# Kernel tuning notes

Measured on AMD Instinct MI355X. Metric: run time of the kernel, lower is better.

## Reference

```python
import jax, jax.numpy as jnp
import numpy as np

# ---- instant-ngp style multi-resolution hash-grid config (matches torch-ngp HashEncoder) ----
NUM_LEVELS = 16
LEVEL_DIM = 2
BASE_RES = 16
DESIRED_RES = 2048
LOG2_T = 19
T_MAX = 2 ** LOG2_T
_pls = np.exp2(np.log2(DESIRED_RES / BASE_RES) / (NUM_LEVELS - 1))  # per-level scale ~1.3819
RESOLUTIONS = [int(np.ceil(BASE_RES * _pls ** l)) for l in range(NUM_LEVELS)]
LEVEL_SIZES = [min(T_MAX, int(np.ceil((r + 1) ** 3 / 8) * 8)) for r in RESOLUTIONS]
OFFSETS = np.concatenate([[0], np.cumsum(LEVEL_SIZES)]).astype(np.int64)
TOTAL_PARAMS = int(OFFSETS[-1])
HASHED = [(r + 1) ** 3 > T_MAX for r in RESOLUTIONS]
CORNERS = np.array([[i, j, k] for i in (0, 1) for j in (0, 1) for k in (0, 1)], dtype=np.float32)  # [8,3]

N_POINTS = 524288
MULTIRES = 6  # positional embedding freqs -> input_ch = 3 + 3*2*6 = 39
D_IN0 = 3 + MULTIRES * 6 + NUM_LEVELS * LEVEL_DIM  # 71


def hash_encode(x, table):
    """x: [N,3] in [0,1]; table: [TOTAL_PARAMS, LEVEL_DIM] -> [N, NUM_LEVELS*LEVEL_DIM]."""
    cn = jnp.asarray(CORNERS)              # [8,3]
    cn_u = cn.astype(jnp.uint32)
    p1, p2, p3 = jnp.uint32(1), jnp.uint32(2654435761), jnp.uint32(805459861)
    outs = []
    for l in range(NUM_LEVELS):
        res = RESOLUTIONS[l]
        pos = x * jnp.float32(res - 1)     # [N,3]
        p0 = jnp.floor(pos)
        w = pos - p0                        # [N,3] trilinear fractions
        cpos = p0.astype(jnp.uint32)[:, None, :] + cn_u[None]  # [N,8,3] corner coords
        if HASHED[l]:
            idx = (cpos[..., 0] * p1) ^ (cpos[..., 1] * p2) ^ (cpos[..., 2] * p3)
            idx = (idx % jnp.uint32(LEVEL_SIZES[l])).astype(jnp.int32)
        else:
            stride = jnp.uint32(res + 1)
            idx = (cpos[..., 0] + cpos[..., 1] * stride + cpos[..., 2] * stride * stride).astype(jnp.int32)
        feats = table[int(OFFSETS[l]) + idx]  # [N,8,LEVEL_DIM] irregular gather
        cw = jnp.where(cn[None] == 1.0, w[:, None, :], 1.0 - w[:, None, :])  # [N,8,3]
        wgt = cw[..., 0] * cw[..., 1] * cw[..., 2]  # [N,8]
        outs.append(jnp.einsum('nc,ncd->nd', wgt, feats))  # [N,LEVEL_DIM]
    return jnp.concatenate(outs, axis=-1)


def pos_embed(x):
    # NeRF embedder, include_input=True, log-sampled freqs 2^0..2^(MULTIRES-1), sin/cos
    freqs = jnp.asarray(2.0 ** np.arange(MULTIRES), dtype=x.dtype)   # [6]
    ang = x[:, None, :] * freqs[None, :, None]                        # [N,6,3]
    sc = jnp.stack([jnp.sin(ang), jnp.cos(ang)], axis=2)              # [N,6,2,3]
    return jnp.concatenate([x, sc.reshape(x.shape[0], -1)], axis=-1)  # [N,39]


def linear_wn(x, v, g, b):
    # nn.utils.weight_norm: W = g * v / ||v||_row
    Wn = v * (g / jnp.linalg.norm(v, axis=1))[:, None]
    return x @ Wn.T + b


def softplus100(x):
    # nn.Softplus(beta=100)
    return jax.nn.softplus(100.0 * x) * 0.01


def setup_inputs() -> dict:
    key = jax.random.key(0)
    ks = jax.random.split(key, 8)
    x = jax.random.uniform(ks[0], (N_POINTS, 3), dtype=jnp.float32)
    hash_table = jax.random.uniform(ks[1], (TOTAL_PARAMS, LEVEL_DIM), jnp.float32, -1e-4, 1e-4)

    def lin(k, dout, din):
        v = jax.random.normal(k, (dout, din), jnp.float32) * jnp.float32(np.sqrt(2.0 / dout))
        g = jnp.linalg.norm(v, axis=1)  # weight_norm init: g = ||v||
        b = jnp.zeros((dout,), jnp.float32)
        return v, g, b

    v0, g0, b0 = lin(ks[2], 256, D_IN0)   # 71 -> 256
    v1, g1, b1 = lin(ks[3], 256, 256)     # 256 -> 256
    v2, g2, b2 = lin(ks[4], 257, 256)     # 256 -> 1 + feature_vector_size
    return {"x": x, "hash_table": hash_table,
            "v0": v0, "g0": g0, "b0": b0,
            "v1": v1, "g1": g1, "b1": b1,
            "v2": v2, "g2": g2, "b2": b2}


def reference(x, hash_table, v0, g0, b0, v1, g1, b1, v2, g2, b2):
    # ImplicitNetworkGrid.forward (divide_factor = 1.0, use_grid_feature = True)
    feat = hash_encode(x, hash_table)                    # [N,32]
    h = jnp.concatenate([pos_embed(x), feat], axis=-1)   # [N,71] = cat(embed, feature)
    h = softplus100(linear_wn(h, v0, g0, b0))
    h = softplus100(linear_wn(h, v1, g1, b1))
    return linear_wn(h, v2, g2, b2)                      # [N,257]: sdf + feature vector
```

## Files before the change

### kernel.cpp

```cpp
#include <hip/hip_runtime.h>
#include <cmath>

typedef float f32x4 __attribute__((ext_vector_type(4)));
typedef short short8 __attribute__((ext_vector_type(8)));

#define N_POINTS 524288
#define TMASK 0x7FFFFu
#define NCELLS 32768

struct HashCfg { int res[16]; int off[16]; unsigned hashed_mask; int total; };

#define S0_OFF   0
#define S1_OFF   1024
#define S2_OFF   2048
#define W2L_OFF  3328
#define B0_OFF   4608
#define B1_OFF   (B0_OFF + 49152)
#define B2_OFF   (B1_OFF + 131072)
#define TBF_OFF  (B2_OFF + 131072)

__device__ inline unsigned short f2bf(float f){
  unsigned u = __float_as_uint(f);
  u = (u + 0x7FFFu + ((u >> 16) & 1u)) >> 16;
  return (unsigned short)u;
}
__device__ inline float bf2f(unsigned short h){
  return __uint_as_float(((unsigned)h) << 16);
}
__device__ inline float softplus100_fast(float x){
  float y = 100.f * x;
  return 0.01f * (fmaxf(y, 0.f) + __logf(1.f + __expf(-fabsf(y))));
}
__device__ inline unsigned morton5(unsigned cx, unsigned cy, unsigned cz){
  unsigned k = 0;
  #pragma unroll
  for (int b = 0; b < 5; b++){
    k |= ((cx >> b) & 1u) << (3*b)
       | ((cy >> b) & 1u) << (3*b + 1)
       | ((cz >> b) & 1u) << (3*b + 2);
  }
  return k;
}

__global__ void scale_kernel(const float* __restrict__ v0, const float* __restrict__ g0,
                             const float* __restrict__ v1, const float* __restrict__ g1,
                             const float* __restrict__ v2, const float* __restrict__ g2,
                             char* __restrict__ ws){
  int r = blockIdx.x * 256 + threadIdx.x;
  if (r < 256){
    float s = 0.f;
    for (int k = 0; k < 71; k++){ float t = v0[r*71+k]; s += t*t; }
    ((float*)(ws + S0_OFF))[r] = g0[r] / sqrtf(s);
  } else if (r < 512){
    int o = r - 256; float s = 0.f;
    for (int k = 0; k < 256; k++){ float t = v1[o*256+k]; s += t*t; }
    ((float*)(ws + S1_OFF))[o] = g1[o] / sqrtf(s);
  } else if (r < 769){
    int o = r - 512; float s = 0.f;
    for (int k = 0; k < 256; k++){ float t = v2[o*256+k]; s += t*t; }
    ((float*)(ws + S2_OFF))[o] = g2[o] / sqrtf(s);
  }
}

__global__ void pack_kernel(const float* __restrict__ v0, const float* __restrict__ v1,
                            const float* __restrict__ v2, char* __restrict__ ws){
  int i = blockIdx.x * 256 + threadIdx.x;
  const float* s0 = (const float*)(ws + S0_OFF);
  const float* s1 = (const float*)(ws + S1_OFF);
  const float* s2 = (const float*)(ws + S2_OFF);
  if (i < 24576){
    int j = i & 7, l = (i >> 3) & 63, q = i >> 9;
    int kt = q % 3, nt = q / 3;
    int k = kt*32 + (l >> 4)*8 + j, col = nt*16 + (l & 15);
    float v = (k < 71) ? v0[col*71 + k] * s0[col] : 0.f;
    ((unsigned short*)(ws + B0_OFF))[i] = f2bf(v);
  } else if (i < 90112){
    int e = i - 24576;
    int j = e & 7, l = (e >> 3) & 63, q = e >> 9;
    int kt = q & 7, nt = q >> 3;
    int k = kt*32 + (l >> 4)*8 + j, col = nt*16 + (l & 15);
    ((unsigned short*)(ws + B1_OFF))[e] = f2bf(v1[col*256 + k] * s1[col]);
  } else if (i < 155648){
    int e = i - 90112;
    int j = e & 7, l = (e >> 3) & 63, q = e >> 9;
    int kt = q & 7, nt = q >> 3;
    int k = kt*32 + (l >> 4)*8 + j, col = nt*16 + (l & 15);
    ((unsigned short*)(ws + B2_OFF))[e] = f2bf(v2[col*256 + k] * s2[col]);
  } else if (i < 155904){
    int k = i - 155648;
    ((float*)(ws + W2L_OFF))[k] = v2[256*256 + k] * s2[256];
  }
}

__global__ void tconv_kernel(const float* __restrict__ table, char* __restrict__ ws, int total){
  int i = blockIdx.x * 256 + threadIdx.x;
  if (i < total){
    float2 v = ((const float2*)table)[i];
    unsigned lo = ((unsigned)f2bf(v.x));
    unsigned hi = ((unsigned)f2bf(v.y)) << 16;
    ((unsigned*)(ws + TBF_OFF))[i] = lo | hi;
  }
}

__global__ void hist_kernel(const float* __restrict__ xin,
                            unsigned* __restrict__ hist, unsigned* __restrict__ keys){
  int i = blockIdx.x * 256 + threadIdx.x;
  float x0 = xin[i*3], x1 = xin[i*3+1], x2 = xin[i*3+2];
  unsigned cx = min(31u, (unsigned)(x0 * 32.f));
  unsigned cy = min(31u, (unsigned)(x1 * 32.f));
  unsigned cz = min(31u, (unsigned)(x2 * 32.f));
  unsigned k = morton5(cx, cy, cz);
  keys[i] = k;
  atomicAdd(&hist[k], 1u);
}

__global__ __launch_bounds__(1024) void scan_kernel(unsigned* __restrict__ hist){
  __shared__ unsigned sdata[1024];
  int t = threadIdx.x;
  unsigned loc[32];
  unsigned s = 0;
  #pragma unroll
  for (int k = 0; k < 32; k++){ loc[k] = hist[t*32 + k]; s += loc[k]; }
  sdata[t] = s;
  __syncthreads();
  for (int d = 1; d < 1024; d <<= 1){
    unsigned v = (t >= d) ? sdata[t - d] : 0u;
    __syncthreads();
    sdata[t] += v;
    __syncthreads();
  }
  unsigned run = (t == 0) ? 0u : sdata[t - 1];
  #pragma unroll
  for (int k = 0; k < 32; k++){ unsigned c = loc[k]; hist[t*32 + k] = run; run += c; }
}

__global__ void scatter_kernel(const unsigned* __restrict__ keys,
                               unsigned* __restrict__ hist, int* __restrict__ perm){
  int i = blockIdx.x * 256 + threadIdx.x;
  unsigned k = keys[i];
  unsigned r = atomicAdd(&hist[k], 1u);
  perm[r] = i;
}

template<int USEBF>
__global__ __launch_bounds__(256, 4) void fused3(
    const float* __restrict__ xin, const float* __restrict__ table,
    char* __restrict__ ws, const int* __restrict__ perm,
    const float* __restrict__ b0, const float* __restrict__ b1, const float* __restrict__ b2,
    float* __restrict__ out, HashCfg cfg)
{
  __shared__ unsigned short buf[64 * 256];
  __shared__ float colsc[4][64];
  __shared__ int pids[64];

  const int tid = threadIdx.x;
  const int p   = tid & 63;
  const int grp = tid >> 6;
  const int lb  = (blockIdx.x & 7) * 1024 + (blockIdx.x >> 3);
  const int idx = lb * 64 + p;
  const int pid = perm ? perm[idx] : idx;
  if (grp == 0) pids[p] = pid;

  const float x0 = xin[pid*3], x1 = xin[pid*3+1], x2 = xin[pid*3+2];
  const unsigned* __restrict__ tbf = (const unsigned*)(ws + TBF_OFF);

  auto stB = [&](int row, int col, float v){
    buf[row*256 + (col ^ ((row & 7) << 3))] = f2bf(v);
  };
  auto ldB = [&](int row, int kb) -> short8 {
    return *(const short8*)&buf[row*256 + (kb ^ ((row & 7) << 3))];
  };

  {
    float wxa[4], wya[4], wza[4];
    unsigned vb[4][8];
    float2   vf2[4][8];

    #pragma unroll
    for (int ii = 0; ii < 4; ii++){
      int lev = grp*4 + ii;
      int res = cfg.res[lev];
      float scl = (float)(res - 1);
      float px = x0*scl, py = x1*scl, pz = x2*scl;
      float fx = floorf(px), fy = floorf(py), fz = floorf(pz);
      wxa[ii] = px - fx; wya[ii] = py - fy; wza[ii] = pz - fz;
      unsigned cx0 = (unsigned)fx, cy0 = (unsigned)fy, cz0 = (unsigned)fz;
      unsigned r1 = (unsigned)(res + 1);
      bool hl = (cfg.hashed_mask >> lev) & 1;
      unsigned base = (unsigned)cfg.off[lev];
      #pragma unroll
      for (int c = 0; c < 8; c++){
        unsigned bx = (c >> 2) & 1, by = (c >> 1) & 1, bz = c & 1;
        unsigned cx = cx0 + bx, cy = cy0 + by, cz = cz0 + bz;
        unsigned hidx = hl ? ((cx ^ (cy * 2654435761u) ^ (cz * 805459861u)) & TMASK)
                           : (cx + cy * r1 + cz * r1 * r1);
        if (USEBF) vb[ii][c]  = tbf[base + hidx];
        else       vf2[ii][c] = *(const float2*)(table + (size_t)(base + hidx) * 2u);
      }
    }

    if (grp < 3){
      float xv[3] = {x0, x1, x2};
      #pragma unroll
      for (int fi = 0; fi < 2; fi++){
        int f = grp*2 + fi;
        float fr = (float)(1 << f);
        #pragma unroll
        for (int d = 0; d < 3; d++){
          float a = xv[d] * fr;
          stB(p, 3 + f*6 + d,     __sinf(a));
          stB(p, 3 + f*6 + 3 + d, __cosf(a));
        }
      }
    } else {
      stB(p, 0, x0); stB(p, 1, x1); stB(p, 2, x2);
      #pragma unroll
      for (int c = 71; c < 96; c++)
        buf[p*256 + (c ^ ((p & 7) << 3))] = 0;
    }

    #pragma unroll
    for (int ii = 0; ii < 4; ii++){
      int lev = grp*4 + ii;
      float wx = wxa[ii], wy = wya[ii], wz = wza[ii];
      float f0 = 0.f, f1 = 0.f;
      #pragma unroll
      for (int c = 0; c < 8; c++){
        unsigned bx = (c >> 2) & 1, by = (c >> 1) & 1, bz = c & 1;
        float w = (bx ? wx : 1.f - wx) * (by ? wy : 1.f - wy) * (bz ? wz : 1.f - wz);
        if (USEBF){
          unsigned u = vb[ii][c];
          f0 += w * __uint_as_float(u << 16);
          f1 += w * __uint_as_float(u & 0xffff0000u);
        } else {
          f0 += w * vf2[ii][c].x;
          f1 += w * vf2[ii][c].y;
        }
      }
      stB(p, 39 + 2*lev, f0);
      stB(p, 40 + 2*lev, f1);
    }
  }
  __syncthreads();

  const int l  = tid & 63;
  const int lr = l & 15;
  const int lh = l >> 4;
  const int wv = grp;
  const short8* B0p = (const short8*)(ws + B0_OFF);
  const short8* B1p = (const short8*)(ws + B1_OFF);
  const short8* B2p = (const short8*)(ws + B2_OFF);

  {
    f32x4 acc[4][4];
    #pragma unroll
    for (int a = 0; a < 4; a++)
      #pragma unroll
      for (int b = 0; b < 4; b++) acc[a][b] = (f32x4){0.f,0.f,0.f,0.f};
    #pragma unroll
    for (int kt = 0; kt < 3; kt++){
      short8 af[4];
      #pragma unroll
      for (int mt = 0; mt < 4; mt++) af[mt] = ldB(mt*16 + lr, kt*32 + lh*8);
      #pragma unroll
      for (int nt = 0; nt < 4; nt++){
        short8 bf = B0p[((wv*4 + nt)*3 + kt)*64 + l];
        #pragma unroll
        for (int mt = 0; mt < 4; mt++)
          acc[mt][nt] = __builtin_amdgcn_mfma_f32_16x16x32_bf16(af[mt], bf, acc[mt][nt], 0, 0, 0);
      }
    }
    __syncthreads();
    float bb[4];
    #pragma unroll
    for (int nt = 0; nt < 4; nt++) bb[nt] = b0[wv*64 + nt*16 + lr];
    #pragma unroll
    for (int mt = 0; mt < 4; mt++)
      #pragma unroll
      for (int nt = 0; nt < 4; nt++){
        int c = wv*64 + nt*16 + lr;
        #pragma unroll
        for (int j = 0; j < 4; j++)
          stB(mt*16 + lh*4 + j, c, softplus100_fast(acc[mt][nt][j] + bb[nt]));
      }
  }
  __syncthreads();

  {
    f32x4 acc[4][4];
    #pragma unroll
    for (int a = 0; a < 4; a++)
      #pragma unroll
      for (int b = 0; b < 4; b++) acc[a][b] = (f32x4){0.f,0.f,0.f,0.f};
    #pragma unroll
    for (int kt = 0; kt < 8; kt++){
      short8 af[4];
      #pragma unroll
      for (int mt = 0; mt < 4; mt++) af[mt] = ldB(mt*16 + lr, kt*32 + lh*8);
      #pragma unroll
      for (int nt = 0; nt < 4; nt++){
        short8 bf = B1p[((wv*4 + nt)*8 + kt)*64 + l];
        #pragma unroll
        for (int mt = 0; mt < 4; mt++)
          acc[mt][nt] = __builtin_amdgcn_mfma_f32_16x16x32_bf16(af[mt], bf, acc[mt][nt], 0, 0, 0);
      }
    }
    __syncthreads();
    float bb[4];
    #pragma unroll
    for (int nt = 0; nt < 4; nt++) bb[nt] = b1[wv*64 + nt*16 + lr];
    #pragma unroll
    for (int mt = 0; mt < 4; mt++)
      #pragma unroll
      for (int nt = 0; nt < 4; nt++){
        int c = wv*64 + nt*16 + lr;
        #pragma unroll
        for (int j = 0; j < 4; j++)
          stB(mt*16 + lh*4 + j, c, softplus100_fast(acc[mt][nt][j] + bb[nt]));
      }
  }
  __syncthreads();

  {
    const float* w2l = (const float*)(ws + W2L_OFF);
    float s = 0.f;
    #pragma unroll
    for (int q = 0; q < 8; q++){
      short8 h = ldB(l, wv*64 + q*8);
      #pragma unroll
      for (int j = 0; j < 8; j++)
        s += bf2f((unsigned short)h[j]) * w2l[wv*64 + q*8 + j];
    }
    colsc[wv][l] = s;
  }

  {
    f32x4 acc[4][4];
    #pragma unroll
    for (int a = 0; a < 4; a++)
      #pragma unroll
      for (int b = 0; b < 4; b++) acc[a][b] = (f32x4){0.f,0.f,0.f,0.f};
    #pragma unroll
    for (int kt = 0; kt < 8; kt++){
      short8 af[4];
      #pragma unroll
      for (int mt = 0; mt < 4; mt++) af[mt] = ldB(mt*16 + lr, kt*32 + lh*8);
      #pragma unroll
      for (int nt = 0; nt < 4; nt++){
        short8 bf = B2p[((wv*4 + nt)*8 + kt)*64 + l];
        #pragma unroll
        for (int mt = 0; mt < 4; mt++)
          acc[mt][nt] = __builtin_amdgcn_mfma_f32_16x16x32_bf16(af[mt], bf, acc[mt][nt], 0, 0, 0);
      }
    }
    __syncthreads();
    float bb[4];
    #pragma unroll
    for (int nt = 0; nt < 4; nt++) bb[nt] = b2[wv*64 + nt*16 + lr];
    int rowid[4][4];
    #pragma unroll
    for (int mt = 0; mt < 4; mt++)
      #pragma unroll
      for (int j = 0; j < 4; j++) rowid[mt][j] = pids[mt*16 + lh*4 + j];
    #pragma unroll
    for (int mt = 0; mt < 4; mt++)
      #pragma unroll
      for (int nt = 0; nt < 4; nt++){
        int c = wv*64 + nt*16 + lr;
        #pragma unroll
        for (int j = 0; j < 4; j++)
          out[(size_t)rowid[mt][j]*257 + c] = acc[mt][nt][j] + bb[nt];
      }
    if (tid < 64)
      out[(size_t)pids[tid]*257 + 256] =
        colsc[0][tid] + colsc[1][tid] + colsc[2][tid] + colsc[3][tid] + b2[256];
  }
}

static HashCfg make_cfg(){
  HashCfg c;
  double pls = exp2(log2(2048.0 / 16.0) / 15.0);
  long long off = 0;
  unsigned mask = 0;
  for (int l = 0; l < 16; l++){
    int r = (int)ceil(16.0 * pow(pls, (double)l));
    c.res[l] = r;
    c.off[l] = (int)off;
    double n3 = (double)(r + 1) * (double)(r + 1) * (double)(r + 1);
    long long size;
    if (n3 > 524288.0){ mask |= (1u << l); }
    size = (long long)(ceil(n3 / 8.0) * 8.0);
    if (size > 524288) size = 524288;
    off += size;
  }
  c.hashed_mask = mask;
  c.total = (int)off;
  return c;
}

extern "C" void kernel_launch(void* const* d_in, const int* in_sizes, int n_in,
                              void* d_out, int out_size, void* d_ws, size_t ws_size,
                              hipStream_t stream) {
  const float* x     = (const float*)d_in[0];
  const float* table = (const float*)d_in[1];
  const float* v0 = (const float*)d_in[2];
  const float* g0 = (const float*)d_in[3];
  const float* b0 = (const float*)d_in[4];
  const float* v1 = (const float*)d_in[5];
  const float* g1 = (const float*)d_in[6];
  const float* b1 = (const float*)d_in[7];
  const float* v2 = (const float*)d_in[8];
  const float* g2 = (const float*)d_in[9];
  const float* b2 = (const float*)d_in[10];
  float* out = (float*)d_out;
  char* ws = (char*)d_ws;

  HashCfg cfg = make_cfg();
  size_t tbf_bytes = (size_t)cfg.total * 4u;
  size_t hist_off  = (TBF_OFF + tbf_bytes + 255) & ~(size_t)255;
  size_t keys_off  = hist_off + (size_t)NCELLS * 4;
  size_t perm_off  = keys_off + (size_t)N_POINTS * 4;
  size_t need_sort = perm_off + (size_t)N_POINTS * 4;
  size_t need_bf   = TBF_OFF + tbf_bytes;

  hipLaunchKernelGGL(scale_kernel, dim3(4), dim3(256), 0, stream, v0, g0, v1, g1, v2, g2, ws);
  hipLaunchKernelGGL(pack_kernel, dim3(609), dim3(256), 0, stream, v0, v1, v2, ws);

  if (ws_size >= need_sort){
    unsigned* hist = (unsigned*)(ws + hist_off);
    unsigned* keys = (unsigned*)(ws + keys_off);
    int*      perm = (int*)(ws + perm_off);
    hipMemsetAsync(hist, 0, (size_t)NCELLS * 4, stream);
    hipLaunchKernelGGL(tconv_kernel, dim3((cfg.total + 255) / 256), dim3(256), 0, stream,
                       table, ws, cfg.total);
    hipLaunchKernelGGL(hist_kernel, dim3(N_POINTS / 256), dim3(256), 0, stream, x, hist, keys);
    hipLaunchKernelGGL(scan_kernel, dim3(1), dim3(1024), 0, stream, hist);
    hipLaunchKernelGGL(scatter_kernel, dim3(N_POINTS / 256), dim3(256), 0, stream, keys, hist, perm);
    hipLaunchKernelGGL((fused3<1>), dim3(N_POINTS / 64), dim3(256), 0, stream,
                       x, table, ws, perm, b0, b1, b2, out, cfg);
  } else if (ws_size >= need_bf){
    hipLaunchKernelGGL(tconv_kernel, dim3((cfg.total + 255) / 256), dim3(256), 0, stream,
                       table, ws, cfg.total);
    hipLaunchKernelGGL((fused3<1>), dim3(N_POINTS / 64), dim3(256), 0, stream,
                       x, table, ws, (const int*)nullptr, b0, b1, b2, out, cfg);
  } else {
    hipLaunchKernelGGL((fused3<0>), dim3(N_POINTS / 64), dim3(256), 0, stream,
                       x, table, ws, (const int*)nullptr, b0, b1, b2, out, cfg);
  }
}
```

Baseline: 789.1 us.

## Process four 64-point tiles per block with prefetched hash gathers

```diff
diff --git a/kernel.cpp b/kernel.cpp
--- a/kernel.cpp
+++ b/kernel.cpp
@@ -7,6 +7,7 @@
 #define N_POINTS 524288
 #define TMASK 0x7FFFFu
 #define NCELLS 32768
+#define TILES  4
 
 struct HashCfg { int res[16]; int off[16]; unsigned hashed_mask; int total; };
 
@@ -96,9 +97,7 @@
   int i = blockIdx.x * 256 + threadIdx.x;
   if (i < total){
     float2 v = ((const float2*)table)[i];
-    unsigned lo = ((unsigned)f2bf(v.x));
-    unsigned hi = ((unsigned)f2bf(v.y)) << 16;
-    ((unsigned*)(ws + TBF_OFF))[i] = lo | hi;
+    ((unsigned*)(ws + TBF_OFF))[i] = ((unsigned)f2bf(v.x)) | (((unsigned)f2bf(v.y)) << 16);
   }
 }
 
@@ -143,7 +142,7 @@
 }
 
 template<int USEBF>
-__global__ __launch_bounds__(256, 4) void fused3(
+__global__ __launch_bounds__(256, 3) void fused4(
     const float* __restrict__ xin, const float* __restrict__ table,
     char* __restrict__ ws, const int* __restrict__ perm,
     const float* __restrict__ b0, const float* __restrict__ b1, const float* __restrict__ b2,
@@ -151,18 +150,23 @@
 {
   __shared__ unsigned short buf[64 * 256];
   __shared__ float colsc[4][64];
-  __shared__ int pids[64];
+  __shared__ int pids_sh[TILES][64];
 
   const int tid = threadIdx.x;
   const int p   = tid & 63;
   const int grp = tid >> 6;
-  const int lb  = (blockIdx.x & 7) * 1024 + (blockIdx.x >> 3);
-  const int idx = lb * 64 + p;
-  const int pid = perm ? perm[idx] : idx;
-  if (grp == 0) pids[p] = pid;
-
-  const float x0 = xin[pid*3], x1 = xin[pid*3+1], x2 = xin[pid*3+2];
+  const int l   = tid & 63;
+  const int lr  = l & 15;
+  const int lh  = l >> 4;
+  const int wv  = grp;
+  const int lb  = (blockIdx.x & 7) * 256 + (blockIdx.x >> 3);
+  const int base_idx = lb * (TILES * 64);
+
   const unsigned* __restrict__ tbf = (const unsigned*)(ws + TBF_OFF);
+  const short8* B0p = (const short8*)(ws + B0_OFF);
+  const short8* B1p = (const short8*)(ws + B1_OFF);
+  const short8* B2p = (const short8*)(ws + B2_OFF);
+  const float* w2l = (const float*)(ws + W2L_OFF);
 
   auto stB = [&](int row, int col, float v){
     buf[row*256 + (col ^ ((row & 7) << 3))] = f2bf(v);
@@ -171,17 +175,29 @@
     return *(const short8*)&buf[row*256 + (kb ^ ((row & 7) << 3))];
   };
 
-  {
-    float wxa[4], wya[4], wza[4];
-    unsigned vb[4][8];
-    float2   vf2[4][8];
-
+  if (grp == 0){
+    #pragma unroll
+    for (int t = 0; t < TILES; t++){
+      int gi = base_idx + t*64 + p;
+      pids_sh[t][p] = perm ? perm[gi] : gi;
+    }
+  }
+  __syncthreads();
+
+  float xc0, xc1, xc2;
+  float wxa[4], wya[4], wza[4];
+  unsigned vb[4][8];
+  float2   vf2[4][8];
+
+  auto issue_tile = [&](int t){
+    int pid = pids_sh[t][p];
+    xc0 = xin[pid*3]; xc1 = xin[pid*3+1]; xc2 = xin[pid*3+2];
     #pragma unroll
     for (int ii = 0; ii < 4; ii++){
       int lev = grp*4 + ii;
       int res = cfg.res[lev];
       float scl = (float)(res - 1);
-      float px = x0*scl, py = x1*scl, pz = x2*scl;
+      float px = xc0*scl, py = xc1*scl, pz = xc2*scl;
       float fx = floorf(px), fy = floorf(py), fz = floorf(pz);
       wxa[ii] = px - fx; wya[ii] = py - fy; wza[ii] = pz - fz;
       unsigned cx0 = (unsigned)fx, cy0 = (unsigned)fy, cz0 = (unsigned)fz;
@@ -198,27 +214,11 @@
         else       vf2[ii][c] = *(const float2*)(table + (size_t)(base + hidx) * 2u);
       }
     }
-
-    if (grp < 3){
-      float xv[3] = {x0, x1, x2};
-      #pragma unroll
-      for (int fi = 0; fi < 2; fi++){
-        int f = grp*2 + fi;
-        float fr = (float)(1 << f);
-        #pragma unroll
-        for (int d = 0; d < 3; d++){
-          float a = xv[d] * fr;
-          stB(p, 3 + f*6 + d,     __sinf(a));
-          stB(p, 3 + f*6 + 3 + d, __cosf(a));
-        }
-      }
-    } else {
-      stB(p, 0, x0); stB(p, 1, x1); stB(p, 2, x2);
-      #pragma unroll
-      for (int c = 71; c < 96; c++)
-        buf[p*256 + (c ^ ((p & 7) << 3))] = 0;
-    }
-
+  };
+
+  issue_tile(0);
+
+  for (int t = 0; t < TILES; t++){
     #pragma unroll
     for (int ii = 0; ii < 4; ii++){
       int lev = grp*4 + ii;
@@ -240,140 +240,152 @@
       stB(p, 39 + 2*lev, f0);
       stB(p, 40 + 2*lev, f1);
     }
-  }
-  __syncthreads();
-
-  const int l  = tid & 63;
-  const int lr = l & 15;
-  const int lh = l >> 4;
-  const int wv = grp;
-  const short8* B0p = (const short8*)(ws + B0_OFF);
-  const short8* B1p = (const short8*)(ws + B1_OFF);
-  const short8* B2p = (const short8*)(ws + B2_OFF);
-
-  {
-    f32x4 acc[4][4];
-    #pragma unroll
-    for (int a = 0; a < 4; a++)
-      #pragma unroll
-      for (int b = 0; b < 4; b++) acc[a][b] = (f32x4){0.f,0.f,0.f,0.f};
-    #pragma unroll
-    for (int kt = 0; kt < 3; kt++){
-      short8 af[4];
-      #pragma unroll
-      for (int mt = 0; mt < 4; mt++) af[mt] = ldB(mt*16 + lr, kt*32 + lh*8);
-      #pragma unroll
-      for (int nt = 0; nt < 4; nt++){
-        short8 bf = B0p[((wv*4 + nt)*3 + kt)*64 + l];
-        #pragma unroll
-        for (int mt = 0; mt < 4; mt++)
-          acc[mt][nt] = __builtin_amdgcn_mfma_f32_16x16x32_bf16(af[mt], bf, acc[mt][nt], 0, 0, 0);
-      }
-    }
+    if (grp < 3){
+      float xv[3] = {xc0, xc1, xc2};
+      #pragma unroll
+      for (int fi = 0; fi < 2; fi++){
+        int f = grp*2 + fi;
+        float fr = (float)(1 << f);
+        #pragma unroll
+        for (int d = 0; d < 3; d++){
+          float a = xv[d] * fr;
+          stB(p, 3 + f*6 + d,     __sinf(a));
+          stB(p, 3 + f*6 + 3 + d, __cosf(a));
+        }
+      }
+    } else {
+      stB(p, 0, xc0); stB(p, 1, xc1); stB(p, 2, xc2);
+      #pragma unroll
+      for (int c = 71; c < 96; c++)
+        buf[p*256 + (c ^ ((p & 7) << 3))] = 0;
+    }
+
+    if (t + 1 < TILES) issue_tile(t + 1);
     __syncthreads();
-    float bb[4];
-    #pragma unroll
-    for (int nt = 0; nt < 4; nt++) bb[nt] = b0[wv*64 + nt*16 + lr];
-    #pragma unroll
-    for (int mt = 0; mt < 4; mt++)
-      #pragma unroll
-      for (int nt = 0; nt < 4; nt++){
-        int c = wv*64 + nt*16 + lr;
-        #pragma unroll
-        for (int j = 0; j < 4; j++)
-          stB(mt*16 + lh*4 + j, c, softplus100_fast(acc[mt][nt][j] + bb[nt]));
-      }
-  }
-  __syncthreads();
-
-  {
-    f32x4 acc[4][4];
-    #pragma unroll
-    for (int a = 0; a < 4; a++)
-      #pragma unroll
-      for (int b = 0; b < 4; b++) acc[a][b] = (f32x4){0.f,0.f,0.f,0.f};
-    #pragma unroll
-    for (int kt = 0; kt < 8; kt++){
-      short8 af[4];
-      #pragma unroll
-      for (int mt = 0; mt < 4; mt++) af[mt] = ldB(mt*16 + lr, kt*32 + lh*8);
-      #pragma unroll
-      for (int nt = 0; nt < 4; nt++){
-        short8 bf = B1p[((wv*4 + nt)*8 + kt)*64 + l];
-        #pragma unroll
-        for (int mt = 0; mt < 4; mt++)
-          acc[mt][nt] = __builtin_amdgcn_mfma_f32_16x16x32_bf16(af[mt], bf, acc[mt][nt], 0, 0, 0);
-      }
+
+    {
+      f32x4 acc[4][4];
+      #pragma unroll
+      for (int a = 0; a < 4; a++)
+        #pragma unroll
+        for (int b = 0; b < 4; b++) acc[a][b] = (f32x4){0.f,0.f,0.f,0.f};
+      #pragma unroll
+      for (int kt = 0; kt < 3; kt++){
+        short8 af[4];
+        #pragma unroll
+        for (int mt = 0; mt < 4; mt++) af[mt] = ldB(mt*16 + lr, kt*32 + lh*8);
+        #pragma unroll
+        for (int nt = 0; nt < 4; nt++){
+          short8 bf = B0p[((wv*4 + nt)*3 + kt)*64 + l];
+          #pragma unroll
+          for (int mt = 0; mt < 4; mt++)
+            acc[mt][nt] = __builtin_amdgcn_mfma_f32_16x16x32_bf16(af[mt], bf, acc[mt][nt], 0, 0, 0);
+        }
+      }
+      __syncthreads();
+      float bb[4];
+      #pragma unroll
+      for (int nt = 0; nt < 4; nt++) bb[nt] = b0[wv*64 + nt*16 + lr];
+      #pragma unroll
+      for (int mt = 0; mt < 4; mt++)
+        #pragma unroll
+        for (int nt = 0; nt < 4; nt++){
+          int c = wv*64 + nt*16 + lr;
+          #pragma unroll
+          for (int j = 0; j < 4; j++)
+            stB(mt*16 + lh*4 + j, c, softplus100_fast(acc[mt][nt][j] + bb[nt]));
+        }
     }
     __syncthreads();
-    float bb[4];
-    #pragma unroll
-    for (int nt = 0; nt < 4; nt++) bb[nt] = b1[wv*64 + nt*16 + lr];
-    #pragma unroll
-    for (int mt = 0; mt < 4; mt++)
-      #pragma unroll
-      for (int nt = 0; nt < 4; nt++){
-        int c = wv*64 + nt*16 + lr;
-        #pragma unroll
-        for (int j = 0; j < 4; j++)
-          stB(mt*16 + lh*4 + j, c, softplus100_fast(acc[mt][nt][j] + bb[nt]));
-      }
-  }
-  __syncthreads();
-
-  {
-    const float* w2l = (const float*)(ws + W2L_OFF);
-    float s = 0.f;
-    #pragma unroll
-    for (int q = 0; q < 8; q++){
-      short8 h = ldB(l, wv*64 + q*8);
-      #pragma unroll
-      for (int j = 0; j < 8; j++)
-        s += bf2f((unsigned short)h[j]) * w2l[wv*64 + q*8 + j];
-    }
-    colsc[wv][l] = s;
-  }
-
-  {
-    f32x4 acc[4][4];
-    #pragma unroll
-    for (int a = 0; a < 4; a++)
-      #pragma unroll
-      for (int b = 0; b < 4; b++) acc[a][b] = (f32x4){0.f,0.f,0.f,0.f};
-    #pragma unroll
-    for (int kt = 0; kt < 8; kt++){
-      short8 af[4];
-      #pragma unroll
-      for (int mt = 0; mt < 4; mt++) af[mt] = ldB(mt*16 + lr, kt*32 + lh*8);
-      #pragma unroll
-      for (int nt = 0; nt < 4; nt++){
-        short8 bf = B2p[((wv*4 + nt)*8 + kt)*64 + l];
-        #pragma unroll
-        for (int mt = 0; mt < 4; mt++)
-          acc[mt][nt] = __builtin_amdgcn_mfma_f32_16x16x32_bf16(af[mt], bf, acc[mt][nt], 0, 0, 0);
-      }
+
+    {
+      f32x4 acc[4][4];
+      #pragma unroll
+      for (int a = 0; a < 4; a++)
+        #pragma unroll
+        for (int b = 0; b < 4; b++) acc[a][b] = (f32x4){0.f,0.f,0.f,0.f};
+      #pragma unroll
+      for (int kt = 0; kt < 8; kt++){
+        short8 af[4];
+        #pragma unroll
+        for (int mt = 0; mt < 4; mt++) af[mt] = ldB(mt*16 + lr, kt*32 + lh*8);
+        #pragma unroll
+        for (int nt = 0; nt < 4; nt++){
+          short8 bf = B1p[((wv*4 + nt)*8 + kt)*64 + l];
+          #pragma unroll
+          for (int mt = 0; mt < 4; mt++)
+            acc[mt][nt] = __builtin_amdgcn_mfma_f32_16x16x32_bf16(af[mt], bf, acc[mt][nt], 0, 0, 0);
+        }
+      }
+      __syncthreads();
+      float bb[4];
+      #pragma unroll
+      for (int nt = 0; nt < 4; nt++) bb[nt] = b1[wv*64 + nt*16 + lr];
+      #pragma unroll
+      for (int mt = 0; mt < 4; mt++)
+        #pragma unroll
+        for (int nt = 0; nt < 4; nt++){
+          int c = wv*64 + nt*16 + lr;
+          #pragma unroll
+          for (int j = 0; j < 4; j++)
+            stB(mt*16 + lh*4 + j, c, softplus100_fast(acc[mt][nt][j] + bb[nt]));
+        }
     }
     __syncthreads();
-    float bb[4];
-    #pragma unroll
-    for (int nt = 0; nt < 4; nt++) bb[nt] = b2[wv*64 + nt*16 + lr];
-    int rowid[4][4];
-    #pragma unroll
-    for (int mt = 0; mt < 4; mt++)
-      #pragma unroll
-      for (int j = 0; j < 4; j++) rowid[mt][j] = pids[mt*16 + lh*4 + j];
-    #pragma unroll
-    for (int mt = 0; mt < 4; mt++)
-      #pragma unroll
-      for (int nt = 0; nt < 4; nt++){
-        int c = wv*64 + nt*16 + lr;
-        #pragma unroll
-        for (int j = 0; j < 4; j++)
-          out[(size_t)rowid[mt][j]*257 + c] = acc[mt][nt][j] + bb[nt];
-      }
-    if (tid < 64)
-      out[(size_t)pids[tid]*257 + 256] =
-        colsc[0][tid] + colsc[1][tid] + colsc[2][tid] + colsc[3][tid] + b2[256];
+
+    {
+      float s = 0.f;
+      #pragma unroll
+      for (int q = 0; q < 8; q++){
+        short8 h = ldB(l, wv*64 + q*8);
+        #pragma unroll
+        for (int j = 0; j < 8; j++)
+          s += bf2f((unsigned short)h[j]) * w2l[wv*64 + q*8 + j];
+      }
+      colsc[wv][l] = s;
+    }
+
+    {
+      f32x4 acc[4][4];
+      #pragma unroll
+      for (int a = 0; a < 4; a++)
+        #pragma unroll
+        for (int b = 0; b < 4; b++) acc[a][b] = (f32x4){0.f,0.f,0.f,0.f};
+      #pragma unroll
+      for (int kt = 0; kt < 8; kt++){
+        short8 af[4];
+        #pragma unroll
+        for (int mt = 0; mt < 4; mt++) af[mt] = ldB(mt*16 + lr, kt*32 + lh*8);
+        #pragma unroll
+        for (int nt = 0; nt < 4; nt++){
+          short8 bf = B2p[((wv*4 + nt)*8 + kt)*64 + l];
+          #pragma unroll
+          for (int mt = 0; mt < 4; mt++)
+            acc[mt][nt] = __builtin_amdgcn_mfma_f32_16x16x32_bf16(af[mt], bf, acc[mt][nt], 0, 0, 0);
+        }
+      }
+      __syncthreads();
+      float bb[4];
+      #pragma unroll
+      for (int nt = 0; nt < 4; nt++) bb[nt] = b2[wv*64 + nt*16 + lr];
+      int rowid[4][4];
+      #pragma unroll
+      for (int mt = 0; mt < 4; mt++)
+        #pragma unroll
+        for (int j = 0; j < 4; j++) rowid[mt][j] = pids_sh[t][mt*16 + lh*4 + j];
+      #pragma unroll
+      for (int mt = 0; mt < 4; mt++)
+        #pragma unroll
+        for (int nt = 0; nt < 4; nt++){
+          int c = wv*64 + nt*16 + lr;
+          #pragma unroll
+          for (int j = 0; j < 4; j++)
+            out[(size_t)rowid[mt][j]*257 + c] = acc[mt][nt][j] + bb[nt];
+        }
+      if (tid < 64)
+        out[(size_t)pids_sh[t][tid]*257 + 256] =
+          colsc[0][tid] + colsc[1][tid] + colsc[2][tid] + colsc[3][tid] + b2[256];
+    }
   }
 }
 
@@ -426,6 +438,8 @@
   hipLaunchKernelGGL(scale_kernel, dim3(4), dim3(256), 0, stream, v0, g0, v1, g1, v2, g2, ws);
   hipLaunchKernelGGL(pack_kernel, dim3(609), dim3(256), 0, stream, v0, v1, v2, ws);
 
+  const int nblk = N_POINTS / (TILES * 64);
+
   if (ws_size >= need_sort){
     unsigned* hist = (unsigned*)(ws + hist_off);
     unsigned* keys = (unsigned*)(ws + keys_off);
@@ -436,15 +450,15 @@
     hipLaunchKernelGGL(hist_kernel, dim3(N_POINTS / 256), dim3(256), 0, stream, x, hist, keys);
     hipLaunchKernelGGL(scan_kernel, dim3(1), dim3(1024), 0, stream, hist);
     hipLaunchKernelGGL(scatter_kernel, dim3(N_POINTS / 256), dim3(256), 0, stream, keys, hist, perm);
-    hipLaunchKernelGGL((fused3<1>), dim3(N_POINTS / 64), dim3(256), 0, stream,
+    hipLaunchKernelGGL((fused4<1>), dim3(nblk), dim3(256), 0, stream,
                        x, table, ws, perm, b0, b1, b2, out, cfg);
   } else if (ws_size >= need_bf){
     hipLaunchKernelGGL(tconv_kernel, dim3((cfg.total + 255) / 256), dim3(256), 0, stream,
                        table, ws, cfg.total);
-    hipLaunchKernelGGL((fused3<1>), dim3(N_POINTS / 64), dim3(256), 0, stream,
+    hipLaunchKernelGGL((fused4<1>), dim3(nblk), dim3(256), 0, stream,
                        x, table, ws, (const int*)nullptr, b0, b1, b2, out, cfg);
   } else {
-    hipLaunchKernelGGL((fused3<0>), dim3(N_POINTS / 64), dim3(256), 0, stream,
+    hipLaunchKernelGGL((fused4<0>), dim3(nblk), dim3(256), 0, stream,
                        x, table, ws, (const int*)nullptr, b0, b1, b2, out, cfg);
   }
 }
```

Result: slower. 2.247 ms (+184.7%).
